# Performance work log

Measured on AMD Instinct MI355X. Metric: run time of the kernel, lower is better.

Reference implementation:

```python
import jax, jax.numpy as jnp
import numpy as np

B, S, D, H, NK = 2, 512, 256, 8, 16
DK = D // H
NEG = -1e32


def _layer_norm(x, g, b, eps=1e-5):
    m = jnp.mean(x, axis=-1, keepdims=True)
    v = jnp.var(x, axis=-1, keepdims=True)
    return (x - m) / jnp.sqrt(v + eps) * g + b


def _attention(q, k, v, mask, gamma, maxout):
    # q,k,v: [b,h,s,dk]; mask: [1,1,s,s] bool; gamma: [h,1,1]
    d_k = q.shape[-1]
    scores = jnp.einsum('bhqd,bhkd->bhqk', q, k) / float(np.sqrt(d_k))
    s = scores.shape[-1]
    # gamma exp-decay branch (at=None in practice -> position_effect path)
    sm = jax.nn.softmax(jnp.where(mask, scores, NEG), axis=-1)
    distcum = jnp.cumsum(sm, axis=-1)
    disttotal = jnp.sum(sm, axis=-1, keepdims=True)
    idx = jnp.arange(s, dtype=scores.dtype)
    pos = jnp.abs(idx[None, :] - idx[:, None])[None, None]  # |x1 - x2|
    dist = jax.lax.stop_gradient(
        jnp.sqrt(jnp.clip((disttotal - distcum) * pos, 0.0, None)))
    g = -jnp.abs(gamma)[None]  # [1,h,1,1]
    total_effect = jnp.clip(jnp.exp(dist * g), 1e-5, 1e5)
    scores = scores * total_effect
    scores = jax.nn.softmax(jnp.where(mask, scores, NEG), axis=-1)
    scores = jnp.where(mask, scores, 0.0)
    if maxout:
        scale = jnp.minimum(1.0 / jnp.max(scores, axis=-1, keepdims=True), 5.0)
        scores = scores * scale
    out = jnp.einsum('bhqk,bhkd->bhqd', scores, v)
    return out, scores


def _mha(qx, kx, vx, mask, Wq, bq, Wk, bk, Wv, bv, Wo, bo, gammas, maxout):
    b, s, d = qx.shape
    def proj(x, W, bb):
        return (x @ W.T + bb).reshape(b, s, H, DK).transpose(0, 2, 1, 3)
    q = proj(qx, Wq, bq)
    k = proj(kx, Wk, bk)
    v = proj(vx, Wv, bv)
    out, scores = _attention(q, k, v, mask, gammas, maxout)
    concat = out.transpose(0, 2, 1, 3).reshape(b, s, d)
    return concat @ Wo.T + bo, scores


def _layer(qx, kx, vx, mask, Wq, bq, Wk, bk, Wv, bv, Wo, bo, gammas, ln_g, ln_b, maxout):
    out, scores = _mha(qx, kx, vx, mask, Wq, bq, Wk, bk, Wv, bv, Wo, bo, gammas, maxout)
    return _layer_norm(qx + out, ln_g, ln_b), scores  # dropout=identity in eval


def setup_inputs() -> dict:
    key = jax.random.key(0)
    ks = iter(jax.random.split(key, 40))
    def W(shp, sc=0.05):
        return jax.random.normal(next(ks), shp, jnp.float32) * sc
    return dict(
        q_emb=jax.random.normal(next(ks), (B, S, D), jnp.float32),
        s_emb=jax.random.normal(next(ks), (B, S, D), jnp.float32),
        s_emb_extr=jax.random.normal(next(ks), (B, S, D), jnp.float32),
        lens=jax.random.randint(next(ks), (B,), 1, S),
        at=jax.random.randint(next(ks), (B, S), 0, 300),
        Wq1=W((D, D)), bq1=jnp.zeros((D,)), Wv1=W((D, D)), bv1=jnp.zeros((D,)),
        Wo1=W((D, D)), bo1=jnp.zeros((D,)), gam1=W((H, 1, 1), 0.3),
        ln1_g=jnp.ones((D,)), ln1_b=jnp.zeros((D,)),
        Wq4=W((D, D)), bq4=jnp.zeros((D,)), Wk4=W((D, D)), bk4=jnp.zeros((D,)),
        Wv4=W((D, D)), bv4=jnp.zeros((D,)),
        Wo4=W((D, D)), bo4=jnp.zeros((D,)), gam4=W((H, 1, 1), 0.3),
        ln4_g=jnp.ones((D,)), ln4_b=jnp.zeros((D,)),
        know_params=jax.random.uniform(next(ks), (NK, D), jnp.float32, -1.0, 1.0),
    )


def reference(q_emb, s_emb, s_emb_extr, lens, at,
              Wq1, bq1, Wv1, bv1, Wo1, bo1, gam1, ln1_g, ln1_b,
              Wq4, bq4, Wk4, bk4, Wv4, bv4, Wo4, bo4, gam4, ln4_g, ln4_b,
              know_params):
    bs, s, d = q_emb.shape
    tri = jnp.tril(jnp.ones((s, s), bool), 0)[None, None]       # peek_cur=True
    tri_strict = jnp.tril(jnp.ones((s, s), bool), -1)[None, None]  # peek_cur=False
    # block1: kq_same -> k_linear is q_linear; maxout=False
    p, q_scores = _layer(q_emb, q_emb, s_emb, tri,
                         Wq1, bq1, Wq1, bq1, Wv1, bv1, Wo1, bo1, gam1,
                         ln1_g, ln1_b, maxout=False)
    # expand knowledge queries: [bs*NK, s, d]
    query = jnp.broadcast_to(know_params[None, :, None, :], (bs, NK, s, d)).reshape(bs * NK, s, d)
    hq = jnp.broadcast_to(q_emb[:, None], (bs, NK, s, d)).reshape(bs * NK, s, d)
    pe = jnp.broadcast_to(p[:, None], (bs, NK, s, d)).reshape(bs * NK, s, d)
    # block4: kq_same=False; maxout=True
    z, k_scores = _layer(query, hq, pe, tri_strict,
                         Wq4, bq4, Wk4, bk4, Wv4, bv4, Wo4, bo4, gam4,
                         ln4_g, ln4_b, maxout=True)
    z = z.reshape(bs, NK, s, d).transpose(0, 2, 1, 3).reshape(bs, s, NK * d)
    k_scores = k_scores.reshape(bs, NK, H, s, s).transpose(0, 2, 3, 1, 4)
    return z, q_scores, k_scores
```

## Files before the change

### kernel.cpp

```cpp
#include <hip/hip_runtime.h>


namespace {
constexpr int kB = 2, kS = 512, kD = 256, kH = 8, kDK = 32, kNK = 16;
constexpr float kScale = 0.17677669529663687f;
constexpr int kPS = 520;
constexpr int kSL = 528;
}

typedef unsigned short u16;
typedef u16 u16x4 __attribute__((ext_vector_type(4)));
typedef u16 u16x8 __attribute__((ext_vector_type(8)));
typedef short s16x8 __attribute__((ext_vector_type(8)));
typedef float f32x4 __attribute__((ext_vector_type(4)));

__device__ __forceinline__ float bf2f(u16 u) { return __uint_as_float(((unsigned)u) << 16); }
__device__ __forceinline__ u16 f2bf(float f) {
    unsigned u = __float_as_uint(f);
    return (u16)((u + 0x7fffu + ((u >> 16) & 1u)) >> 16);
}

__device__ __forceinline__ float wave_max64(float v) {
#pragma unroll
    for (int off = 32; off; off >>= 1) v = fmaxf(v, __shfl_xor(v, off));
    return v;
}
__device__ __forceinline__ float wave_sum64(float v) {
#pragma unroll
    for (int off = 32; off; off >>= 1) v += __shfl_xor(v, off);
    return v;
}

__global__ __launch_bounds__(256) void wt_kernel(const float* __restrict__ W0,
                                                 const float* __restrict__ W1,
                                                 const float* __restrict__ W2,
                                                 const float* __restrict__ W3,
                                                 const float* __restrict__ W4,
                                                 const float* __restrict__ W5,
                                                 float* __restrict__ WT) {
    __shared__ float tile[32][33];
    const float* srcs[6] = {W0, W1, W2, W3, W4, W5};
    const float* W = srcs[blockIdx.y];
    float* T = WT + (size_t)blockIdx.y * kD * kD;
    const int tx = blockIdx.x & 7, ty = blockIdx.x >> 3;
    const int t = threadIdx.x;
    {
        const int cl = t >> 3, kl = (t & 7) * 4;
        f32x4 v = *(const f32x4*)(W + (size_t)(ty * 32 + cl) * kD + tx * 32 + kl);
        tile[cl][kl] = v[0]; tile[cl][kl + 1] = v[1];
        tile[cl][kl + 2] = v[2]; tile[cl][kl + 3] = v[3];
    }
    __syncthreads();
    {
        const int kl = t >> 3, cl = (t & 7) * 4;
        f32x4 o = {tile[cl][kl], tile[cl + 1][kl], tile[cl + 2][kl], tile[cl + 3][kl]};
        *(f32x4*)(T + (size_t)(tx * 32 + kl) * kD + ty * 32 + cl) = o;
    }
}

__global__ __launch_bounds__(256) void vt4_kernel(const float* __restrict__ V4,
                                                  u16* __restrict__ Vtg) {
    __shared__ float tile[128][33];
    const int bh = blockIdx.x, kt = blockIdx.y;
    const int t = threadIdx.x;
    const float* src = V4 + ((size_t)bh * kS + kt * 128) * kDK;
    for (int i = t * 4; i < 128 * 32; i += 1024) {
        f32x4 v = *(const f32x4*)(src + i);
        const int k = i >> 5, d = i & 31;
        tile[k][d] = v[0]; tile[k][d + 1] = v[1];
        tile[k][d + 2] = v[2]; tile[k][d + 3] = v[3];
    }
    __syncthreads();
    const int d = t >> 3, kc = (t & 7) * 16;
    u16* dst = Vtg + ((size_t)bh * kDK + d) * kS + kt * 128 + kc;
    u16x8 o1, o2;
#pragma unroll
    for (int j = 0; j < 8; ++j) o1[j] = f2bf(tile[kc + j][d]);
#pragma unroll
    for (int j = 0; j < 8; ++j) o2[j] = f2bf(tile[kc + 8 + j][d]);
    *(u16x8*)dst = o1;
    *(u16x8*)(dst + 8) = o2;
}

template <int RPW, int MODE>
__global__ __launch_bounds__(256) void gemm256(const float* __restrict__ X,
                                               const float* __restrict__ WT,
                                               const float* __restrict__ bias,
                                               const float* __restrict__ extra,
                                               const float* __restrict__ lng,
                                               const float* __restrict__ lnb,
                                               float* __restrict__ Y) {
    constexpr int TM = RPW * 4;
    __shared__ float xs[TM][kD];
    const int t = threadIdx.x;
    const int r0 = blockIdx.x * TM;

    if (MODE == 0) {
#pragma unroll
        for (int it = 0; it < RPW; ++it) {
            const int idx = it * 1024 + t * 4;
            const int r = idx >> 8, c = idx & 255;
            *(f32x4*)&xs[r][c] = *(const f32x4*)(X + (size_t)(r0 + r) * kD + c);
        }
    } else {
#pragma unroll
        for (int it = 0; it < RPW; ++it) {
            const int chunk = it * 32 + (t >> 3);
            const int r = chunk >> 3, h = chunk & 7;
            const int row = r0 + r;
            const float* src = X + (((size_t)(row >> 9) * kH + h) * kS + (row & (kS - 1))) * kDK + (t & 7) * 4;
            *(f32x4*)&xs[r][h * kDK + (t & 7) * 4] = *(const f32x4*)src;
        }
    }
    __syncthreads();

    const int wv = t >> 6;
    const int c4 = (t & 63) * 4;
    float acc[RPW][4];
    {
        f32x4 bv = *(const f32x4*)(bias + c4);
#pragma unroll
        for (int r = 0; r < RPW; ++r)
#pragma unroll
            for (int j = 0; j < 4; ++j) acc[r][j] = bv[j];
    }
    for (int k0 = 0; k0 < kD; k0 += 4) {
        f32x4 w0 = *(const f32x4*)(WT + (size_t)(k0 + 0) * kD + c4);
        f32x4 w1 = *(const f32x4*)(WT + (size_t)(k0 + 1) * kD + c4);
        f32x4 w2 = *(const f32x4*)(WT + (size_t)(k0 + 2) * kD + c4);
        f32x4 w3 = *(const f32x4*)(WT + (size_t)(k0 + 3) * kD + c4);
#pragma unroll
        for (int r = 0; r < RPW; ++r) {
            f32x4 xv = *(const f32x4*)&xs[wv * RPW + r][k0];
#pragma unroll
            for (int cc = 0; cc < 4; ++cc) {
                acc[r][cc] = fmaf(xv[0], w0[cc], acc[r][cc]);
                acc[r][cc] = fmaf(xv[1], w1[cc], acc[r][cc]);
                acc[r][cc] = fmaf(xv[2], w2[cc], acc[r][cc]);
                acc[r][cc] = fmaf(xv[3], w3[cc], acc[r][cc]);
            }
        }
    }

#pragma unroll
    for (int r = 0; r < RPW; ++r) {
        const int row = r0 + wv * RPW + r;
        if (MODE == 0) {
            const int h = c4 >> 5, dk = c4 & 31;
            *(f32x4*)(Y + (((size_t)(row >> 9) * kH + h) * kS + (row & (kS - 1))) * kDK + dk) =
                *(f32x4*)acc[r];
        } else {
            f32x4 x;
            if (MODE == 1) {
                f32x4 e = *(const f32x4*)(extra + (size_t)row * kD + c4);
#pragma unroll
                for (int j = 0; j < 4; ++j) x[j] = acc[r][j] + e[j];
            } else {
                const int nk = (row >> 9) & (kNK - 1);
                f32x4 e = *(const f32x4*)(extra + (size_t)nk * kD + c4);
#pragma unroll
                for (int j = 0; j < 4; ++j) x[j] = acc[r][j] + e[j];
            }
            float s1 = x[0] + x[1] + x[2] + x[3];
            float s2 = x[0] * x[0] + x[1] * x[1] + x[2] * x[2] + x[3] * x[3];
#pragma unroll
            for (int off = 32; off; off >>= 1) {
                s1 += __shfl_xor(s1, off);
                s2 += __shfl_xor(s2, off);
            }
            const float mean = s1 * (1.f / kD);
            const float var = s2 * (1.f / kD) - mean * mean;
            const float rstd = rsqrtf(var + 1e-5f);
            f32x4 g = *(const f32x4*)(lng + c4);
            f32x4 bb = *(const f32x4*)(lnb + c4);
            f32x4 y;
#pragma unroll
            for (int j = 0; j < 4; ++j) y[j] = (x[j] - mean) * rstd * g[j] + bb[j];
            if (MODE == 1) {
                *(f32x4*)(Y + (size_t)row * kD + c4) = y;
            } else {
                const int bnk = row >> 9, s = row & (kS - 1);
                const int nk = bnk & (kNK - 1), b = bnk >> 4;
                *(f32x4*)(Y + (((size_t)(b * kS + s) * kNK + nk) * kD) + c4) = y;
            }
        }
    }
}

__global__ __launch_bounds__(256) void gemm256_b3(const float* __restrict__ X0,
                                                  const float* __restrict__ WT0,
                                                  const float* __restrict__ b0,
                                                  float* __restrict__ Y0,
                                                  const float* __restrict__ X1,
                                                  const float* __restrict__ WT1,
                                                  const float* __restrict__ b1,
                                                  float* __restrict__ Y1,
                                                  const float* __restrict__ X2,
                                                  const float* __restrict__ WT2,
                                                  const float* __restrict__ b2,
                                                  float* __restrict__ Y2) {
    __shared__ float xs[4][kD];
    const float* X = (blockIdx.y == 0) ? X0 : (blockIdx.y == 1) ? X1 : X2;
    const float* WT = (blockIdx.y == 0) ? WT0 : (blockIdx.y == 1) ? WT1 : WT2;
    const float* bias = (blockIdx.y == 0) ? b0 : (blockIdx.y == 1) ? b1 : b2;
    float* Y = (blockIdx.y == 0) ? Y0 : (blockIdx.y == 1) ? Y1 : Y2;
    const int t = threadIdx.x;
    const int r0 = blockIdx.x * 4;

    {
        const int idx = t * 4;
        const int r = idx >> 8, c = idx & 255;
        *(f32x4*)&xs[r][c] = *(const f32x4*)(X + (size_t)(r0 + r) * kD + c);
    }
    __syncthreads();

    const int wv = t >> 6;
    const int c4 = (t & 63) * 4;
    float acc[4];
    {
        f32x4 bv = *(const f32x4*)(bias + c4);
#pragma unroll
        for (int j = 0; j < 4; ++j) acc[j] = bv[j];
    }
    for (int k0 = 0; k0 < kD; k0 += 4) {
        f32x4 w0 = *(const f32x4*)(WT + (size_t)(k0 + 0) * kD + c4);
        f32x4 w1 = *(const f32x4*)(WT + (size_t)(k0 + 1) * kD + c4);
        f32x4 w2 = *(const f32x4*)(WT + (size_t)(k0 + 2) * kD + c4);
        f32x4 w3 = *(const f32x4*)(WT + (size_t)(k0 + 3) * kD + c4);
        f32x4 xv = *(const f32x4*)&xs[wv][k0];
#pragma unroll
        for (int cc = 0; cc < 4; ++cc) {
            acc[cc] = fmaf(xv[0], w0[cc], acc[cc]);
            acc[cc] = fmaf(xv[1], w1[cc], acc[cc]);
            acc[cc] = fmaf(xv[2], w2[cc], acc[cc]);
            acc[cc] = fmaf(xv[3], w3[cc], acc[cc]);
        }
    }
    const int row = r0 + wv;
    const int h = c4 >> 5, dk = c4 & 31;
    *(f32x4*)(Y + (((size_t)(row >> 9) * kH + h) * kS + (row & (kS - 1))) * kDK + dk) =
        *(f32x4*)acc;
}

__global__ __launch_bounds__(256) void proj_kernel(const float* __restrict__ X,
                                                   const float* __restrict__ W,
                                                   const float* __restrict__ bias,
                                                   float* __restrict__ Y, int scatter) {
    const int row = blockIdx.x;
    const int c = threadIdx.x;
    __shared__ float xs[kD];
    xs[c] = X[(size_t)row * kD + c];
    __syncthreads();
    float acc = bias[c];
    const float* wr = W + (size_t)c * kD;
#pragma unroll 4
    for (int k0 = 0; k0 < kD; k0 += 4) {
        f32x4 wv = *(const f32x4*)(wr + k0);
#pragma unroll
        for (int j = 0; j < 4; ++j) acc = fmaf(xs[k0 + j], wv[j], acc);
    }
    if (scatter) {
        const int b = row >> 9, s = row & (kS - 1);
        const int h = c >> 5, dk = c & 31;
        Y[((size_t)(b * kH + h) * kS + s) * kDK + dk] = acc;
    } else {
        Y[(size_t)row * kD + c] = acc;
    }
}

__global__ __launch_bounds__(256) void attn1_kernel(const float* __restrict__ Q1,
                                                    const u16* __restrict__ Vtg1,
                                                    const float* __restrict__ gam,
                                                    float* __restrict__ q_scores,
                                                    float* __restrict__ A1) {
    extern __shared__ char smem[];
    float* Sl = (float*)smem;
    u16* Pl = (u16*)smem;

    const int bh = blockIdx.x;
    const int q0 = blockIdx.y * 16;
    const int h = bh & (kH - 1);
    const int tid = threadIdx.x;
    const int lane = tid & 63;
    const int w = tid >> 6;
    const float* Kb = Q1 + (size_t)bh * kS * kDK;

    {
        const int qrow = q0 + (lane & 15);
        const int dof = (lane >> 4) * 8;
        f32x4 qa = *(const f32x4*)(Kb + (size_t)qrow * kDK + dof);
        f32x4 qb = *(const f32x4*)(Kb + (size_t)qrow * kDK + dof + 4);
        s16x8 aq_h, aq_l;
#pragma unroll
        for (int j = 0; j < 4; ++j) {
            float f = qa[j];
            u16 hi = f2bf(f);
            aq_h[j] = (short)hi;
            aq_l[j] = (short)f2bf(f - bf2f(hi));
            f = qb[j];
            hi = f2bf(f);
            aq_h[4 + j] = (short)hi;
            aq_l[4 + j] = (short)f2bf(f - bf2f(hi));
        }
        for (int kt = w * 8; kt < w * 8 + 8; ++kt) {
            const int krow = kt * 16 + (lane & 15);
            f32x4 ka = *(const f32x4*)(Kb + (size_t)krow * kDK + dof);
            f32x4 kb2 = *(const f32x4*)(Kb + (size_t)krow * kDK + dof + 4);
            s16x8 bk_h, bk_l;
#pragma unroll
            for (int j = 0; j < 4; ++j) {
                float f = ka[j];
                u16 hi = f2bf(f);
                bk_h[j] = (short)hi;
                bk_l[j] = (short)f2bf(f - bf2f(hi));
                f = kb2[j];
                hi = f2bf(f);
                bk_h[4 + j] = (short)hi;
                bk_l[4 + j] = (short)f2bf(f - bf2f(hi));
            }
            f32x4 acc = {0.f, 0.f, 0.f, 0.f};
            acc = __builtin_amdgcn_mfma_f32_16x16x32_bf16(aq_h, bk_h, acc, 0, 0, 0);
            acc = __builtin_amdgcn_mfma_f32_16x16x32_bf16(aq_l, bk_h, acc, 0, 0, 0);
            acc = __builtin_amdgcn_mfma_f32_16x16x32_bf16(aq_h, bk_l, acc, 0, 0, 0);
            const int colk = kt * 16 + (lane & 15);
            const int seg = colk >> 5, ii = colk & 31;
#pragma unroll
            for (int j = 0; j < 4; ++j) {
                const int row = (lane >> 4) * 4 + j;
                Sl[row * kSL + seg * 33 + ii] = acc[j] * kScale;
            }
        }
    }
    __syncthreads();

    const float gh = -fabsf(gam[h]);
    const int r = tid >> 4, seg16 = tid & 15;
    const int q = q0 + r, L = q + 1, ks = seg16 * 32;
    float sv[32];
    {
        const float* srow = Sl + r * kSL + seg16 * 33;
#pragma unroll
        for (int i = 0; i < 32; ++i) sv[i] = srow[i];
    }
    __syncthreads();
    {
        const int nv = min(max(L - ks, 0), 32);
        float m = -3e38f;
#pragma unroll
        for (int i = 0; i < 32; ++i)
            if (i < nv) m = fmaxf(m, sv[i]);
#pragma unroll
        for (int off = 1; off < 16; off <<= 1) m = fmaxf(m, __shfl_xor(m, off));
        float segsum = 0.f;
#pragma unroll
        for (int i = 0; i < 32; ++i)
            if (i < nv) segsum += __expf(sv[i] - m);
        float tot = segsum;
#pragma unroll
        for (int off = 1; off < 16; off <<= 1) tot += __shfl_xor(tot, off);
        float inc = segsum;
#pragma unroll
        for (int off = 1; off < 16; off <<= 1) {
            const float tmp = __shfl_up(inc, off);
            if ((tid & 15) >= off) inc += tmp;
        }
        float run = inc - segsum;
        const float inv_tot = 1.f / tot;
        float m2 = -3e38f;
#pragma unroll
        for (int i = 0; i < 32; ++i) {
            if (i < nv) {
                const float E = __expf(sv[i] - m);
                run += E;
                const float rem = 1.f - run * inv_tot;
                const float pos = (float)(q - (ks + i));
                const float val = fmaxf(rem * pos, 0.f);
                const float te = fmaxf(__expf(gh * sqrtf(val)), 1e-5f);
                const float s2 = sv[i] * te;
                sv[i] = s2;
                m2 = fmaxf(m2, s2);
            }
        }
#pragma unroll
        for (int off = 1; off < 16; off <<= 1) m2 = fmaxf(m2, __shfl_xor(m2, off));
        float sum2 = 0.f;
#pragma unroll
        for (int i = 0; i < 32; ++i) {
            const float p = (i < nv) ? __expf(sv[i] - m2) : 0.f;
            sv[i] = p;
            sum2 += p;
        }
#pragma unroll
        for (int off = 1; off < 16; off <<= 1) sum2 += __shfl_xor(sum2, off);
        const float inv2 = 1.f / sum2;
        float* qrow = q_scores + ((size_t)bh * kS + q) * kS + ks;
        u16* prow = Pl + r * kPS + ks;
#pragma unroll
        for (int i = 0; i < 32; i += 4) {
            f32x4 o;
            u16x4 pb;
#pragma unroll
            for (int j = 0; j < 4; ++j) {
                const float p = sv[i + j] * inv2;
                o[j] = p;
                pb[j] = f2bf(p);
            }
            *(f32x4*)(qrow + i) = o;
            *(u16x4*)(prow + i) = pb;
        }
    }
    __syncthreads();

    if (w < 2) {
        const int dt = w;
        const u16* Arow = Pl + (size_t)(lane & 15) * kPS + (lane >> 4) * 8;
        const u16* Brow = Vtg1 + ((size_t)bh * kDK + dt * 16 + (lane & 15)) * kS + (lane >> 4) * 8;
        f32x4 acc = {0.f, 0.f, 0.f, 0.f};
#pragma unroll
        for (int kc = 0; kc < kS; kc += 32) {
            s16x8 a = *(const s16x8*)(Arow + kc);
            s16x8 b = *(const s16x8*)(Brow + kc);
            acc = __builtin_amdgcn_mfma_f32_16x16x32_bf16(a, b, acc, 0, 0, 0);
        }
        const int d = dt * 16 + (lane & 15);
#pragma unroll
        for (int j = 0; j < 4; ++j) {
            const int row = (lane >> 4) * 4 + j;
            A1[((size_t)bh * kS + (q0 + row)) * kDK + d] = acc[j];
        }
    }
}

__global__ __launch_bounds__(64) void attn4_prep(const float* __restrict__ Q4,
                                                 const float* __restrict__ K4,
                                                 float* __restrict__ rawP,
                                                 float* __restrict__ CpreP) {
    const int panel = blockIdx.x;
    const int h = panel & (kH - 1);
    const int bnk = panel >> 3;
    const int nk = bnk & (kNK - 1);
    const int b = bnk >> 4;
    const int lane = threadIdx.x;
    const float* Kp = K4 + (size_t)(b * kH + h) * kS * kDK;
    float qv[kDK];
    const float* Qr = Q4 + (size_t)nk * kD + h * kDK;
#pragma unroll
    for (int d = 0; d < kDK; ++d) qv[d] = Qr[d];

    const int k0 = lane * 8;
    float raw[8];
    float m = -3e38f;
#pragma unroll
    for (int j = 0; j < 8; ++j) {
        const float* kr = Kp + (size_t)(k0 + j) * kDK;
        float s = 0.f;
#pragma unroll
        for (int d4 = 0; d4 < 8; ++d4) {
            f32x4 kv = *(const f32x4*)(kr + d4 * 4);
            s = fmaf(qv[d4 * 4 + 0], kv[0], s);
            s = fmaf(qv[d4 * 4 + 1], kv[1], s);
            s = fmaf(qv[d4 * 4 + 2], kv[2], s);
            s = fmaf(qv[d4 * 4 + 3], kv[3], s);
        }
        raw[j] = s * kScale;
        m = fmaxf(m, raw[j]);
    }
    m = wave_max64(m);
    float E[8];
    float s = 0.f;
#pragma unroll
    for (int j = 0; j < 8; ++j) { E[j] = __expf(raw[j] - m); s += E[j]; }
    float inc = s;
#pragma unroll
    for (int off = 1; off < 64; off <<= 1) {
        float t = __shfl_up(inc, off);
        if (lane >= off) inc += t;
    }
    float run = inc - s;
    float cp[8];
#pragma unroll
    for (int j = 0; j < 8; ++j) { run += E[j]; cp[j] = run; }

    float* rrow = rawP + (size_t)panel * kS + k0;
    float* crow = CpreP + (size_t)panel * kS + k0;
    *(f32x4*)(rrow) = *(f32x4*)(raw);
    *(f32x4*)(rrow + 4) = *(f32x4*)(raw + 4);
    *(f32x4*)(crow) = *(f32x4*)(cp);
    *(f32x4*)(crow + 4) = *(f32x4*)(cp + 4);
}

__global__ __launch_bounds__(256) void attn4_main(const float* __restrict__ rawP,
                                                  const float* __restrict__ CpreP,
                                                  const u16* __restrict__ Vtg,
                                                  const float* __restrict__ gam,
                                                  float* __restrict__ k_scores,
                                                  float* __restrict__ A4) {
    extern __shared__ char smem[];
    u16* Pl = (u16*)smem;
    float* raws_l = (float*)(smem + 32 * kPS * 2);
    float* cps_l = raws_l + kS;

    const int panel = blockIdx.x;
    const int q0 = blockIdx.y * 32;
    const int h = panel & (kH - 1);
    const int bnk = panel >> 3;
    const int nk = bnk & (kNK - 1);
    const int b = bnk >> 4;
    const int tid = threadIdx.x;
    const int lane = tid & 63;
    const int w = tid >> 6;

    for (int i = tid; i < kS; i += 256) {
        raws_l[i] = rawP[(size_t)panel * kS + i];
        cps_l[i] = CpreP[(size_t)panel * kS + i];
    }
    __syncthreads();

    const float gh = -fabsf(gam[h]);
    const int rbase = w * 8;
    const int k0 = lane * 8;
    float rw[8], cp[8];
    *(f32x4*)(rw) = *(const f32x4*)(raws_l + k0);
    *(f32x4*)(rw + 4) = *(const f32x4*)(raws_l + k0 + 4);
    *(f32x4*)(cp) = *(const f32x4*)(cps_l + k0);
    *(f32x4*)(cp + 4) = *(const f32x4*)(cps_l + k0 + 4);

    for (int r = 0; r < 8; ++r) {
        const int row = rbase + r;
        const int Lr = q0 + row;
        float* krow = k_scores + ((size_t)((b * kH + h) * kS + Lr) * kNK + nk) * kS;
        u16* prow = Pl + (size_t)row * kPS + k0;
        if (Lr == 0) {
            f32x4 z = {0.f, 0.f, 0.f, 0.f};
            *(f32x4*)(krow + k0) = z;
            *(f32x4*)(krow + k0 + 4) = z;
            u16x8 zb = {0, 0, 0, 0, 0, 0, 0, 0};
            *(u16x8*)(prow) = zb;
            continue;
        }
        const float invCL = 1.f / cps_l[Lr - 1];
        const float fL = (float)(Lr - k0);
        float s2v[8];
        float mloc = -3e38f;
#pragma unroll
        for (int j = 0; j < 8; ++j) {
            const float rem = 1.f - cp[j] * invCL;
            const float val = fmaxf(rem * (fL - (float)j), 0.f);
            const float te = fmaxf(__expf(gh * sqrtf(val)), 1e-5f);
            const float s2 = rw[j] * te;
            s2v[j] = s2;
            if (k0 + j < Lr) mloc = fmaxf(mloc, s2);
        }
        const float m2 = wave_max64(mloc);
        float p[8];
        float psum = 0.f;
#pragma unroll
        for (int j = 0; j < 8; ++j) {
            p[j] = (k0 + j < Lr) ? __expf(s2v[j] - m2) : 0.f;
            psum += p[j];
        }
        const float sum2 = wave_sum64(psum);
        const float scl = fminf(sum2, 5.f) / sum2;
        u16x8 pb;
#pragma unroll
        for (int j = 0; j < 8; ++j) {
            p[j] *= scl;
            pb[j] = f2bf(p[j]);
        }
        *(f32x4*)(krow + k0) = *(f32x4*)(p);
        *(f32x4*)(krow + k0 + 4) = *(f32x4*)(p + 4);
        *(u16x8*)(prow) = pb;
    }
    __syncthreads();

    const int rowblk = (w & 1) * 16;
    const int dblk = (w >> 1) * 16;
    const u16* Arow = Pl + (size_t)(rowblk + (lane & 15)) * kPS + (lane >> 4) * 8;
    const u16* Brow = Vtg + ((size_t)(b * kH + h) * kDK + dblk + (lane & 15)) * kS + (lane >> 4) * 8;
    f32x4 acc = {0.f, 0.f, 0.f, 0.f};
#pragma unroll
    for (int kc = 0; kc < kS; kc += 32) {
        s16x8 a = *(const s16x8*)(Arow + kc);
        s16x8 bfr = *(const s16x8*)(Brow + kc);
        acc = __builtin_amdgcn_mfma_f32_16x16x32_bf16(a, bfr, acc, 0, 0, 0);
    }
    const int d = dblk + (lane & 15);
#pragma unroll
    for (int j = 0; j < 4; ++j) {
        const int row = rowblk + (lane >> 4) * 4 + j;
        A4[((size_t)panel * kS + (q0 + row)) * kDK + d] = acc[j];
    }
}

extern "C" void kernel_launch(void* const* d_in, const int* in_sizes, int n_in,
                              void* d_out, int out_size, void* d_ws, size_t ws_size,
                              hipStream_t stream) {
    (void)in_sizes; (void)n_in; (void)out_size; (void)ws_size;

    const float* q_emb = (const float*)d_in[0];
    const float* s_emb = (const float*)d_in[1];
    const float* Wq1 = (const float*)d_in[5];  const float* bq1 = (const float*)d_in[6];
    const float* Wv1 = (const float*)d_in[7];  const float* bv1 = (const float*)d_in[8];
    const float* Wo1 = (const float*)d_in[9];  const float* bo1 = (const float*)d_in[10];
    const float* gam1 = (const float*)d_in[11];
    const float* ln1g = (const float*)d_in[12]; const float* ln1b = (const float*)d_in[13];
    const float* Wq4 = (const float*)d_in[14]; const float* bq4 = (const float*)d_in[15];
    const float* Wk4 = (const float*)d_in[16]; const float* bk4 = (const float*)d_in[17];
    const float* Wv4 = (const float*)d_in[18]; const float* bv4 = (const float*)d_in[19];
    const float* Wo4 = (const float*)d_in[20]; const float* bo4 = (const float*)d_in[21];
    const float* gam4 = (const float*)d_in[22];
    const float* ln4g = (const float*)d_in[23]; const float* ln4b = (const float*)d_in[24];
    const float* know = (const float*)d_in[25];

    float* ws = (float*)d_ws;
    const size_t NBHSD = (size_t)kB * kH * kS * kDK;
    float* Q1 = ws;
    float* V1 = Q1 + NBHSD;
    float* A1 = V1 + NBHSD;
    float* P  = A1 + NBHSD;
    float* K4 = P  + (size_t)kB * kS * kD;
    float* V4 = K4 + NBHSD;
    float* Q4 = V4 + NBHSD;
    float* A4 = Q4 + (size_t)kNK * kD;
    float* WT = A4 + (size_t)kB * kNK * kH * kS * kDK;
    u16* Vtg = (u16*)(WT + 6 * (size_t)kD * kD);
    u16* Vtg1 = Vtg + (size_t)kB * kH * kDK * kS;

    float* rawP = V1;
    float* CpreP = V1 + (size_t)kB * kNK * kH * kS;

    float* WTq1 = WT + 0 * (size_t)kD * kD;
    float* WTv1 = WT + 1 * (size_t)kD * kD;
    float* WTo1 = WT + 2 * (size_t)kD * kD;
    float* WTk4 = WT + 3 * (size_t)kD * kD;
    float* WTv4 = WT + 4 * (size_t)kD * kD;
    float* WTo4 = WT + 5 * (size_t)kD * kD;

    float* zout = (float*)d_out;
    float* q_scores = zout + (size_t)kB * kS * kNK * kD;
    float* k_scores = q_scores + (size_t)kB * kH * kS * kS;

    {
        dim3 g(64, 6);
        wt_kernel<<<g, 256, 0, stream>>>(Wq1, Wv1, Wo1, Wk4, Wv4, Wo4, WT);
    }
    {
        dim3 g(kB * kS / 4, 3);
        gemm256_b3<<<g, 256, 0, stream>>>(q_emb, WTq1, bq1, Q1,
                                          s_emb, WTv1, bv1, V1,
                                          q_emb, WTk4, bk4, K4);
    }
    proj_kernel<<<kNK, 256, 0, stream>>>(know, Wq4, bq4, Q4, 0);
    {
        dim3 gv(kB * kH, 4);
        vt4_kernel<<<gv, 256, 0, stream>>>(V1, Vtg1);
    }

    {
        dim3 g1(kB * kH, kS / 16);
        const int lds1 = 16 * kSL * 4;
        attn1_kernel<<<g1, 256, lds1, stream>>>(Q1, Vtg1, gam1, q_scores, A1);
    }
    gemm256<1, 1><<<kB * kS / 4, 256, 0, stream>>>(A1, WTo1, bo1, q_emb, ln1g, ln1b, P);

    gemm256<1, 0><<<kB * kS / 4, 256, 0, stream>>>(P, WTv4, bv4, nullptr, nullptr, nullptr, V4);
    {
        dim3 gv(kB * kH, 4);
        vt4_kernel<<<gv, 256, 0, stream>>>(V4, Vtg);
    }
    attn4_prep<<<kB * kNK * kH, 64, 0, stream>>>(Q4, K4, rawP, CpreP);
    {
        dim3 g5(kB * kNK * kH, kS / 32);
        const int lds_bytes = 32 * kPS * 2 + 2 * kS * 4;
        attn4_main<<<g5, 256, lds_bytes, stream>>>(rawP, CpreP, Vtg, gam4, k_scores, A4);
    }
    gemm256<4, 2><<<kB * kNK * kS / 16, 256, 0, stream>>>(A4, WTo4, bo4, know, ln4g, ln4b, zout);
}
```

Measured before the change: 230.7 us.

## Fuse projection kernels and write transposed bf16 V directly, cutting launches

Merges the Q1/V1/K4 projections and the knowledge-query projection into one four-mode kernel, with the V projection writing the transposed bf16 layout directly so the separate transpose kernels go away. The Wo1+residual+LayerNorm epilogue and the V4 projection are fused into one kernel that keeps P in shared memory and writes the transposed bf16 V4. This removes several launches and intermediate global round-trips (V1, P, V4). In exchange it adds strided 2-byte scattered stores and an idle early-exit grid slice.

```diff
diff --git a/kernel.cpp b/kernel.cpp
--- a/kernel.cpp
+++ b/kernel.cpp
@@ -37,9 +37,10 @@
                                                  const float* __restrict__ W3,
                                                  const float* __restrict__ W4,
                                                  const float* __restrict__ W5,
+                                                 const float* __restrict__ W6,
                                                  float* __restrict__ WT) {
     __shared__ float tile[32][33];
-    const float* srcs[6] = {W0, W1, W2, W3, W4, W5};
+    const float* srcs[7] = {W0, W1, W2, W3, W4, W5, W6};
     const float* W = srcs[blockIdx.y];
     float* T = WT + (size_t)blockIdx.y * kD * kD;
     const int tx = blockIdx.x & 7, ty = blockIdx.x >> 3;
@@ -58,28 +59,168 @@
     }
 }
 
-__global__ __launch_bounds__(256) void vt4_kernel(const float* __restrict__ V4,
-                                                  u16* __restrict__ Vtg) {
-    __shared__ float tile[128][33];
-    const int bh = blockIdx.x, kt = blockIdx.y;
+__global__ __launch_bounds__(256) void gemm256_b4(const float* __restrict__ q_emb,
+                                                  const float* __restrict__ s_emb,
+                                                  const float* __restrict__ know,
+                                                  const float* __restrict__ WTq1,
+                                                  const float* __restrict__ bq1,
+                                                  const float* __restrict__ WTv1,
+                                                  const float* __restrict__ bv1,
+                                                  const float* __restrict__ WTk4,
+                                                  const float* __restrict__ bk4,
+                                                  const float* __restrict__ WTq4,
+                                                  const float* __restrict__ bq4,
+                                                  float* __restrict__ Q1,
+                                                  u16* __restrict__ Vtg1,
+                                                  float* __restrict__ K4,
+                                                  float* __restrict__ Q4) {
+    const int mode = blockIdx.y;
+    if (mode == 3 && blockIdx.x >= 4) return;
+    __shared__ float xs[4][kD];
+    const float* X = (mode == 1) ? s_emb : (mode == 3) ? know : q_emb;
+    const float* WT = (mode == 0) ? WTq1 : (mode == 1) ? WTv1 : (mode == 2) ? WTk4 : WTq4;
+    const float* bias = (mode == 0) ? bq1 : (mode == 1) ? bv1 : (mode == 2) ? bk4 : bq4;
     const int t = threadIdx.x;
-    const float* src = V4 + ((size_t)bh * kS + kt * 128) * kDK;
-    for (int i = t * 4; i < 128 * 32; i += 1024) {
-        f32x4 v = *(const f32x4*)(src + i);
-        const int k = i >> 5, d = i & 31;
-        tile[k][d] = v[0]; tile[k][d + 1] = v[1];
-        tile[k][d + 2] = v[2]; tile[k][d + 3] = v[3];
-    }
-    __syncthreads();
-    const int d = t >> 3, kc = (t & 7) * 16;
-    u16* dst = Vtg + ((size_t)bh * kDK + d) * kS + kt * 128 + kc;
-    u16x8 o1, o2;
-#pragma unroll
-    for (int j = 0; j < 8; ++j) o1[j] = f2bf(tile[kc + j][d]);
-#pragma unroll
-    for (int j = 0; j < 8; ++j) o2[j] = f2bf(tile[kc + 8 + j][d]);
-    *(u16x8*)dst = o1;
-    *(u16x8*)(dst + 8) = o2;
+    const int r0 = blockIdx.x * 4;
+
+    {
+        const int idx = t * 4;
+        const int r = idx >> 8, c = idx & 255;
+        *(f32x4*)&xs[r][c] = *(const f32x4*)(X + (size_t)(r0 + r) * kD + c);
+    }
+    __syncthreads();
+
+    const int wv = t >> 6;
+    const int c4 = (t & 63) * 4;
+    float acc[4];
+    {
+        f32x4 bv = *(const f32x4*)(bias + c4);
+#pragma unroll
+        for (int j = 0; j < 4; ++j) acc[j] = bv[j];
+    }
+    for (int k0 = 0; k0 < kD; k0 += 4) {
+        f32x4 w0 = *(const f32x4*)(WT + (size_t)(k0 + 0) * kD + c4);
+        f32x4 w1 = *(const f32x4*)(WT + (size_t)(k0 + 1) * kD + c4);
+        f32x4 w2 = *(const f32x4*)(WT + (size_t)(k0 + 2) * kD + c4);
+        f32x4 w3 = *(const f32x4*)(WT + (size_t)(k0 + 3) * kD + c4);
+        f32x4 xv = *(const f32x4*)&xs[wv][k0];
+#pragma unroll
+        for (int cc = 0; cc < 4; ++cc) {
+            acc[cc] = fmaf(xv[0], w0[cc], acc[cc]);
+            acc[cc] = fmaf(xv[1], w1[cc], acc[cc]);
+            acc[cc] = fmaf(xv[2], w2[cc], acc[cc]);
+            acc[cc] = fmaf(xv[3], w3[cc], acc[cc]);
+        }
+    }
+    const int row = r0 + wv;
+    if (mode == 3) {
+        *(f32x4*)(Q4 + (size_t)row * kD + c4) = *(f32x4*)acc;
+    } else if (mode == 1) {
+        const int b = row >> 9, s = row & (kS - 1);
+        const int h = c4 >> 5, dk = c4 & 31;
+        u16* base = Vtg1 + (((size_t)(b * kH + h) * kDK + dk) * kS + s);
+#pragma unroll
+        for (int j = 0; j < 4; ++j) base[(size_t)j * kS] = f2bf(acc[j]);
+    } else {
+        float* Y = (mode == 0) ? Q1 : K4;
+        const int h = c4 >> 5, dk = c4 & 31;
+        *(f32x4*)(Y + (((size_t)(row >> 9) * kH + h) * kS + (row & (kS - 1))) * kDK + dk) =
+            *(f32x4*)acc;
+    }
+}
+
+__global__ __launch_bounds__(256) void epi1v4_kernel(const float* __restrict__ A1,
+                                                     const float* __restrict__ qe,
+                                                     const float* __restrict__ WTo1,
+                                                     const float* __restrict__ bo1,
+                                                     const float* __restrict__ lng,
+                                                     const float* __restrict__ lnb,
+                                                     const float* __restrict__ WTv4,
+                                                     const float* __restrict__ bv4,
+                                                     u16* __restrict__ Vtg) {
+    __shared__ float xs[4][kD];
+    __shared__ float ps[4][kD];
+    const int t = threadIdx.x;
+    const int r0 = blockIdx.x * 4;
+
+    {
+        const int chunk = t >> 3;
+        const int r = chunk >> 3, h = chunk & 7;
+        const int row = r0 + r;
+        const float* src = A1 + (((size_t)(row >> 9) * kH + h) * kS + (row & (kS - 1))) * kDK + (t & 7) * 4;
+        *(f32x4*)&xs[r][h * kDK + (t & 7) * 4] = *(const f32x4*)src;
+    }
+    __syncthreads();
+
+    const int wv = t >> 6;
+    const int c4 = (t & 63) * 4;
+    const int row = r0 + wv;
+
+    {
+        float acc[4];
+        f32x4 bv = *(const f32x4*)(bo1 + c4);
+#pragma unroll
+        for (int j = 0; j < 4; ++j) acc[j] = bv[j];
+        for (int k0 = 0; k0 < kD; k0 += 4) {
+            f32x4 w0 = *(const f32x4*)(WTo1 + (size_t)(k0 + 0) * kD + c4);
+            f32x4 w1 = *(const f32x4*)(WTo1 + (size_t)(k0 + 1) * kD + c4);
+            f32x4 w2 = *(const f32x4*)(WTo1 + (size_t)(k0 + 2) * kD + c4);
+            f32x4 w3 = *(const f32x4*)(WTo1 + (size_t)(k0 + 3) * kD + c4);
+            f32x4 xv = *(const f32x4*)&xs[wv][k0];
+#pragma unroll
+            for (int cc = 0; cc < 4; ++cc) {
+                acc[cc] = fmaf(xv[0], w0[cc], acc[cc]);
+                acc[cc] = fmaf(xv[1], w1[cc], acc[cc]);
+                acc[cc] = fmaf(xv[2], w2[cc], acc[cc]);
+                acc[cc] = fmaf(xv[3], w3[cc], acc[cc]);
+            }
+        }
+        f32x4 e = *(const f32x4*)(qe + (size_t)row * kD + c4);
+        f32x4 x;
+#pragma unroll
+        for (int j = 0; j < 4; ++j) x[j] = acc[j] + e[j];
+        float s1 = x[0] + x[1] + x[2] + x[3];
+        float s2 = x[0] * x[0] + x[1] * x[1] + x[2] * x[2] + x[3] * x[3];
+#pragma unroll
+        for (int off = 32; off; off >>= 1) {
+            s1 += __shfl_xor(s1, off);
+            s2 += __shfl_xor(s2, off);
+        }
+        const float mean = s1 * (1.f / kD);
+        const float var = s2 * (1.f / kD) - mean * mean;
+        const float rstd = rsqrtf(var + 1e-5f);
+        f32x4 g = *(const f32x4*)(lng + c4);
+        f32x4 bb = *(const f32x4*)(lnb + c4);
+#pragma unroll
+        for (int j = 0; j < 4; ++j) ps[wv][c4 + j] = (x[j] - mean) * rstd * g[j] + bb[j];
+    }
+    __syncthreads();
+
+    {
+        float acc[4];
+        f32x4 bv = *(const f32x4*)(bv4 + c4);
+#pragma unroll
+        for (int j = 0; j < 4; ++j) acc[j] = bv[j];
+        for (int k0 = 0; k0 < kD; k0 += 4) {
+            f32x4 w0 = *(const f32x4*)(WTv4 + (size_t)(k0 + 0) * kD + c4);
+            f32x4 w1 = *(const f32x4*)(WTv4 + (size_t)(k0 + 1) * kD + c4);
+            f32x4 w2 = *(const f32x4*)(WTv4 + (size_t)(k0 + 2) * kD + c4);
+            f32x4 w3 = *(const f32x4*)(WTv4 + (size_t)(k0 + 3) * kD + c4);
+            f32x4 xv = *(const f32x4*)&ps[wv][k0];
+#pragma unroll
+            for (int cc = 0; cc < 4; ++cc) {
+                acc[cc] = fmaf(xv[0], w0[cc], acc[cc]);
+                acc[cc] = fmaf(xv[1], w1[cc], acc[cc]);
+                acc[cc] = fmaf(xv[2], w2[cc], acc[cc]);
+                acc[cc] = fmaf(xv[3], w3[cc], acc[cc]);
+            }
+        }
+        const int b = row >> 9, s = row & (kS - 1);
+        const int h = c4 >> 5, dk = c4 & 31;
+        u16* base = Vtg + (((size_t)(b * kH + h) * kDK + dk) * kS + s);
+#pragma unroll
+        for (int j = 0; j < 4; ++j) base[(size_t)j * kS] = f2bf(acc[j]);
+    }
 }
 
 template <int RPW, int MODE>
@@ -184,87 +325,6 @@
                 *(f32x4*)(Y + (((size_t)(b * kS + s) * kNK + nk) * kD) + c4) = y;
             }
         }
-    }
-}
-
-__global__ __launch_bounds__(256) void gemm256_b3(const float* __restrict__ X0,
-                                                  const float* __restrict__ WT0,
-                                                  const float* __restrict__ b0,
-                                                  float* __restrict__ Y0,
-                                                  const float* __restrict__ X1,
-                                                  const float* __restrict__ WT1,
-                                                  const float* __restrict__ b1,
-                                                  float* __restrict__ Y1,
-                                                  const float* __restrict__ X2,
-                                                  const float* __restrict__ WT2,
-                                                  const float* __restrict__ b2,
-                                                  float* __restrict__ Y2) {
-    __shared__ float xs[4][kD];
-    const float* X = (blockIdx.y == 0) ? X0 : (blockIdx.y == 1) ? X1 : X2;
-    const float* WT = (blockIdx.y == 0) ? WT0 : (blockIdx.y == 1) ? WT1 : WT2;
-    const float* bias = (blockIdx.y == 0) ? b0 : (blockIdx.y == 1) ? b1 : b2;
-    float* Y = (blockIdx.y == 0) ? Y0 : (blockIdx.y == 1) ? Y1 : Y2;
-    const int t = threadIdx.x;
-    const int r0 = blockIdx.x * 4;
-
-    {
-        const int idx = t * 4;
-        const int r = idx >> 8, c = idx & 255;
-        *(f32x4*)&xs[r][c] = *(const f32x4*)(X + (size_t)(r0 + r) * kD + c);
-    }
-    __syncthreads();
-
-    const int wv = t >> 6;
-    const int c4 = (t & 63) * 4;
-    float acc[4];
-    {
-        f32x4 bv = *(const f32x4*)(bias + c4);
-#pragma unroll
-        for (int j = 0; j < 4; ++j) acc[j] = bv[j];
-    }
-    for (int k0 = 0; k0 < kD; k0 += 4) {
-        f32x4 w0 = *(const f32x4*)(WT + (size_t)(k0 + 0) * kD + c4);
-        f32x4 w1 = *(const f32x4*)(WT + (size_t)(k0 + 1) * kD + c4);
-        f32x4 w2 = *(const f32x4*)(WT + (size_t)(k0 + 2) * kD + c4);
-        f32x4 w3 = *(const f32x4*)(WT + (size_t)(k0 + 3) * kD + c4);
-        f32x4 xv = *(const f32x4*)&xs[wv][k0];
-#pragma unroll
-        for (int cc = 0; cc < 4; ++cc) {
-            acc[cc] = fmaf(xv[0], w0[cc], acc[cc]);
-            acc[cc] = fmaf(xv[1], w1[cc], acc[cc]);
-            acc[cc] = fmaf(xv[2], w2[cc], acc[cc]);
-            acc[cc] = fmaf(xv[3], w3[cc], acc[cc]);
-        }
-    }
-    const int row = r0 + wv;
-    const int h = c4 >> 5, dk = c4 & 31;
-    *(f32x4*)(Y + (((size_t)(row >> 9) * kH + h) * kS + (row & (kS - 1))) * kDK + dk) =
-        *(f32x4*)acc;
-}
-
-__global__ __launch_bounds__(256) void proj_kernel(const float* __restrict__ X,
-                                                   const float* __restrict__ W,
-                                                   const float* __restrict__ bias,
-                                                   float* __restrict__ Y, int scatter) {
-    const int row = blockIdx.x;
-    const int c = threadIdx.x;
-    __shared__ float xs[kD];
-    xs[c] = X[(size_t)row * kD + c];
-    __syncthreads();
-    float acc = bias[c];
-    const float* wr = W + (size_t)c * kD;
-#pragma unroll 4
-    for (int k0 = 0; k0 < kD; k0 += 4) {
-        f32x4 wv = *(const f32x4*)(wr + k0);
-#pragma unroll
-        for (int j = 0; j < 4; ++j) acc = fmaf(xs[k0 + j], wv[j], acc);
-    }
-    if (scatter) {
-        const int b = row >> 9, s = row & (kS - 1);
-        const int h = c >> 5, dk = c & 31;
-        Y[((size_t)(b * kH + h) * kS + s) * kDK + dk] = acc;
-    } else {
-        Y[(size_t)row * kD + c] = acc;
     }
 }
 
@@ -615,19 +675,17 @@
     float* ws = (float*)d_ws;
     const size_t NBHSD = (size_t)kB * kH * kS * kDK;
     float* Q1 = ws;
-    float* V1 = Q1 + NBHSD;
-    float* A1 = V1 + NBHSD;
-    float* P  = A1 + NBHSD;
-    float* K4 = P  + (size_t)kB * kS * kD;
-    float* V4 = K4 + NBHSD;
-    float* Q4 = V4 + NBHSD;
+    float* RAW = Q1 + NBHSD;
+    float* A1 = RAW + NBHSD;
+    float* K4 = A1 + NBHSD;
+    float* Q4 = K4 + NBHSD;
     float* A4 = Q4 + (size_t)kNK * kD;
     float* WT = A4 + (size_t)kB * kNK * kH * kS * kDK;
-    u16* Vtg = (u16*)(WT + 6 * (size_t)kD * kD);
+    u16* Vtg = (u16*)(WT + 7 * (size_t)kD * kD);
     u16* Vtg1 = Vtg + (size_t)kB * kH * kDK * kS;
 
-    float* rawP = V1;
-    float* CpreP = V1 + (size_t)kB * kNK * kH * kS;
+    float* rawP = RAW;
+    float* CpreP = RAW + (size_t)kB * kNK * kH * kS;
 
     float* WTq1 = WT + 0 * (size_t)kD * kD;
     float* WTv1 = WT + 1 * (size_t)kD * kD;
@@ -635,40 +693,30 @@
     float* WTk4 = WT + 3 * (size_t)kD * kD;
     float* WTv4 = WT + 4 * (size_t)kD * kD;
     float* WTo4 = WT + 5 * (size_t)kD * kD;
+    float* WTq4 = WT + 6 * (size_t)kD * kD;
 
     float* zout = (float*)d_out;
     float* q_scores = zout + (size_t)kB * kS * kNK * kD;
     float* k_scores = q_scores + (size_t)kB * kH * kS * kS;
 
     {
-        dim3 g(64, 6);
-        wt_kernel<<<g, 256, 0, stream>>>(Wq1, Wv1, Wo1, Wk4, Wv4, Wo4, WT);
-    }
-    {
-        dim3 g(kB * kS / 4, 3);
-        gemm256_b3<<<g, 256, 0, stream>>>(q_emb, WTq1, bq1, Q1,
-                                          s_emb, WTv1, bv1, V1,
-                                          q_emb, WTk4, bk4, K4);
-    }
-    proj_kernel<<<kNK, 256, 0, stream>>>(know, Wq4, bq4, Q4, 0);
-    {
-        dim3 gv(kB * kH, 4);
-        vt4_kernel<<<gv, 256, 0, stream>>>(V1, Vtg1);
-    }
-
+        dim3 g(64, 7);
+        wt_kernel<<<g, 256, 0, stream>>>(Wq1, Wv1, Wo1, Wk4, Wv4, Wo4, Wq4, WT);
+    }
+    {
+        dim3 g(kB * kS / 4, 4);
+        gemm256_b4<<<g, 256, 0, stream>>>(q_emb, s_emb, know,
+                                          WTq1, bq1, WTv1, bv1, WTk4, bk4, WTq4, bq4,
+                                          Q1, Vtg1, K4, Q4);
+    }
+    attn4_prep<<<kB * kNK * kH, 64, 0, stream>>>(Q4, K4, rawP, CpreP);
     {
         dim3 g1(kB * kH, kS / 16);
         const int lds1 = 16 * kSL * 4;
         attn1_kernel<<<g1, 256, lds1, stream>>>(Q1, Vtg1, gam1, q_scores, A1);
     }
-    gemm256<1, 1><<<kB * kS / 4, 256, 0, stream>>>(A1, WTo1, bo1, q_emb, ln1g, ln1b, P);
-
-    gemm256<1, 0><<<kB * kS / 4, 256, 0, stream>>>(P, WTv4, bv4, nullptr, nullptr, nullptr, V4);
-    {
-        dim3 gv(kB * kH, 4);
-        vt4_kernel<<<gv, 256, 0, stream>>>(V4, Vtg);
-    }
-    attn4_prep<<<kB * kNK * kH, 64, 0, stream>>>(Q4, K4, rawP, CpreP);
+    epi1v4_kernel<<<kB * kS / 4, 256, 0, stream>>>(A1, q_emb, WTo1, bo1, ln1g, ln1b,
+                                                   WTv4, bv4, Vtg);
     {
         dim3 g5(kB * kNK * kH, kS / 32);
         const int lds_bytes = 32 * kPS * 2 + 2 * kS * 4;
```

New measurement: 218.7 us. 5.2% less time.
